# Kernel tuning notes

Measured on AMD Instinct MI355X. Metric: run time of the kernel, lower is better.

## Reference

```python
import jax, jax.numpy as jnp
import numpy as np

B, T, D, E = 4, 8192, 2048, 64


def setup_inputs() -> dict:
    key = jax.random.key(0)
    k1, k2 = jax.random.split(key)
    x = jax.random.normal(k1, (B, T, D), dtype=jnp.float32)
    kernel_DE = jax.random.normal(k2, (D, E), dtype=jnp.float32) * 0.02
    return {"x": x, "kernel_DE": kernel_DE, "num_experts_per_tok": 8}


def reference(x, kernel_DE, num_experts_per_tok):
    dtype = x.dtype
    # router logits: (B,T,E)
    router_logits_BTE = jnp.einsum("BTD,DE->BTE", x, kernel_DE)
    # gating probs in fp32 for numerical stability
    activated_gating_BTE = jax.nn.softmax(router_logits_BTE.astype(jnp.float32), axis=-1)
    # top-k experts per token
    weights_BTX, selected_experts_BTX = jax.lax.top_k(activated_gating_BTE, num_experts_per_tok)
    # renormalize selected weights via softmax in model dtype (faithful to source)
    normalized_weights_BTX = jax.nn.softmax(weights_BTX.astype(dtype), axis=-1)
    return (normalized_weights_BTX, selected_experts_BTX)
```

## Files before the change

### kernel.cpp

```cpp
#include <hip/hip_runtime.h>
#include <math.h>

#define NTOK  32768
#define DDIM  2048
#define NEXP  64
#define TOPK  8
#define GAP_THR  1e-4f
#define LIST_CAP 16384

#define WFRAG_OFF  1024
#define WFRAG_SZ   (64 * 4 * 2048)
#define LIST_OFF   (WFRAG_OFF + WFRAG_SZ)

#define CK      2
#define NCHUNK  (DDIM / 32 / CK)

typedef __attribute__((ext_vector_type(8))) short s8_t;
typedef __attribute__((ext_vector_type(4))) float f4_t;
typedef __attribute__((ext_vector_type(4))) unsigned int u4_t;

typedef const __attribute__((address_space(1))) unsigned int* as1p;
typedef __attribute__((address_space(3))) unsigned int* as3p;

__device__ __forceinline__ void gl2lds16(const void* g, void* l) {
  __builtin_amdgcn_global_load_lds((as1p)g, (as3p)l, 16, 0, 0);
}

__device__ __forceinline__ unsigned short f2bf(float f) {
  const unsigned u = __builtin_bit_cast(unsigned, f);
  const unsigned r = u + 0x7FFFu + ((u >> 16) & 1u);
  return (unsigned short)(r >> 16);
}

struct bfpair { unsigned hi, lo; };
__device__ __forceinline__ bfpair split2(float a, float b) {
  const unsigned ua = __builtin_bit_cast(unsigned, a);
  const unsigned ub = __builtin_bit_cast(unsigned, b);
  const unsigned ra = ua + 0x7FFFu + ((ua >> 16) & 1u);
  const unsigned rb = ub + 0x7FFFu + ((ub >> 16) & 1u);
  bfpair r;
  r.hi = (ra >> 16) | (rb & 0xFFFF0000u);
  const float fa = a - __builtin_bit_cast(float, ra & 0xFFFF0000u);
  const float fb = b - __builtin_bit_cast(float, rb & 0xFFFF0000u);
  r.lo = (__builtin_bit_cast(unsigned, fa) >> 16) |
         (__builtin_bit_cast(unsigned, fb) & 0xFFFF0000u);
  return r;
}

__global__ void wprep(const float* __restrict__ w, unsigned short* __restrict__ wf,
                      int* __restrict__ cnt) {
  if (blockIdx.x == 0 && threadIdx.x == 0) cnt[0] = 0;
  const int ks   = blockIdx.x;
  const int eg   = threadIdx.x >> 6;
  const int lane = threadIdx.x & 63;
  const int kb   = ks * 32 + ((lane >> 4) << 3);
  const int e    = (eg << 4) + (lane & 15);
  s8_t h, l;
#pragma unroll
  for (int j = 0; j < 8; ++j) {
    const float v = w[(size_t)(kb + j) * NEXP + e];
    const unsigned short hb = f2bf(v);
    const float hf = __builtin_bit_cast(float, (unsigned)hb << 16);
    h[j] = (short)hb;
    l[j] = (short)f2bf(v - hf);
  }
  unsigned short* base = wf + (size_t)(ks * 4 + eg) * 1024 + lane * 8;
  *(s8_t*)(base)       = h;
  *(s8_t*)(base + 512) = l;
}

__global__ __launch_bounds__(256, 2) void router_main(
    const float* __restrict__ x, const unsigned short* __restrict__ wfg,
    float* __restrict__ out, int* __restrict__ cnt, int* __restrict__ list) {
  __shared__ union {
    struct {
      float xb[2][4][CK * 512];
      unsigned short wb[2][CK * 4096];
    } s;
    float ll[64 * 68];
  } u;

  const int tid  = threadIdx.x;
  const int lane = tid & 63;
  const int wave = tid >> 6;
  const int col  = lane & 15;
  const int kgrp = lane >> 4;
  const int wtok = blockIdx.x * 64 + wave * 16;

  f4_t acc[4];
#pragma unroll
  for (int eg = 0; eg < 4; ++eg) acc[eg] = (f4_t){0.f, 0.f, 0.f, 0.f};

  const float* gx0 = x + (size_t)(wtok + col) * DDIM + (kgrp << 3);

  {
    float* lx = &u.s.xb[0][wave][0];
#pragma unroll
    for (int kk = 0; kk < CK; ++kk) {
      gl2lds16(gx0 + kk * 32,     lx + kk * 512);
      gl2lds16(gx0 + kk * 32 + 4, lx + kk * 512 + 256);
    }
    const unsigned short* gw = wfg + wave * 2048 + lane * 8;
    unsigned short* lw = &u.s.wb[0][wave * 2048];
#pragma unroll
    for (int j = 0; j < 4; ++j)
      gl2lds16(gw + j * 512, lw + j * 512);
  }
  __syncthreads();

#pragma unroll 1
  for (int c = 0; c < NCHUNK; ++c) {
    const int b = c & 1;
    if (c + 1 < NCHUNK) {
      const int nb = b ^ 1;
      const float* gx = gx0 + (size_t)((c + 1) * CK) * 32;
      float* lx = &u.s.xb[nb][wave][0];
#pragma unroll
      for (int kk = 0; kk < CK; ++kk) {
        gl2lds16(gx + kk * 32,     lx + kk * 512);
        gl2lds16(gx + kk * 32 + 4, lx + kk * 512 + 256);
      }
      const unsigned short* gw =
          wfg + (size_t)((c + 1) * CK) * 4096 + wave * 2048 + lane * 8;
      unsigned short* lw = &u.s.wb[nb][wave * 2048];
#pragma unroll
      for (int j = 0; j < 4; ++j)
        gl2lds16(gw + j * 512, lw + j * 512);
    }

    const float* lx = &u.s.xb[b][wave][0];
    const unsigned short* lw = &u.s.wb[b][0];
#pragma unroll
    for (int kk = 0; kk < CK; ++kk) {
      const float4 v0 = *(const float4*)(lx + kk * 512 + lane * 4);
      const float4 v1 = *(const float4*)(lx + kk * 512 + 256 + lane * 4);
      const bfpair p0 = split2(v0.x, v0.y);
      const bfpair p1 = split2(v0.z, v0.w);
      const bfpair p2 = split2(v1.x, v1.y);
      const bfpair p3 = split2(v1.z, v1.w);
      const u4_t uh = {p0.hi, p1.hi, p2.hi, p3.hi};
      const u4_t ul = {p0.lo, p1.lo, p2.lo, p3.lo};
      const s8_t ah = __builtin_bit_cast(s8_t, uh);
      const s8_t al = __builtin_bit_cast(s8_t, ul);
#pragma unroll
      for (int eg = 0; eg < 4; ++eg) {
        const s8_t bh = *(const s8_t*)(lw + kk * 4096 + eg * 1024 + lane * 8);
        const s8_t bl = *(const s8_t*)(lw + kk * 4096 + eg * 1024 + 512 + lane * 8);
        acc[eg] = __builtin_amdgcn_mfma_f32_16x16x32_bf16(ah, bh, acc[eg], 0, 0, 0);
        acc[eg] = __builtin_amdgcn_mfma_f32_16x16x32_bf16(al, bh, acc[eg], 0, 0, 0);
        acc[eg] = __builtin_amdgcn_mfma_f32_16x16x32_bf16(ah, bl, acc[eg], 0, 0, 0);
      }
    }
    __syncthreads();
  }

#pragma unroll
  for (int eg = 0; eg < 4; ++eg)
#pragma unroll
    for (int r = 0; r < 4; ++r)
      u.ll[(wave * 16 + kgrp * 4 + r) * 68 + eg * 16 + col] = acc[eg][r];
  __syncthreads();

  float* out_w = out;
  float* out_i = out + (size_t)NTOK * TOPK;

#pragma unroll 1
  for (int t = 0; t < 16; ++t) {
    const int tok = wtok + t;
    const float v = u.ll[(wave * 16 + t) * 68 + lane];

    float m = v;
#pragma unroll
    for (int off = 32; off; off >>= 1) m = fmaxf(m, __shfl_xor(m, off));
    const float ex = __expf(v - m);
    float s = ex;
#pragma unroll
    for (int off = 32; off; off >>= 1) s += __shfl_xor(s, off);
    float pw = ex / s;
    float lw = v;
    int   ii = lane;

    float selp[TOPK + 1];
    float sell[TOPK + 1];
    int   seli[TOPK + 1];
#pragma unroll
    for (int r = 0; r < TOPK + 1; ++r) {
      float bp = pw; float bl = lw; int bi = ii;
#pragma unroll
      for (int off = 32; off; off >>= 1) {
        const float op = __shfl_xor(bp, off);
        const float ol = __shfl_xor(bl, off);
        const int   oi = __shfl_xor(bi, off);
        const bool take = (op > bp) || (op == bp && oi < bi);
        bp = take ? op : bp;
        bl = take ? ol : bl;
        bi = take ? oi : bi;
      }
      selp[r] = bp; sell[r] = bl; seli[r] = bi;
      if (lane == bi) pw = -__builtin_inff();
    }

    bool contested = false;
#pragma unroll
    for (int k = 0; k < TOPK; ++k)
      contested |= (sell[k] - sell[k + 1]) <= GAP_THR;

    const float mm = selp[0];
    float ssum = 0.0f;
#pragma unroll
    for (int k = 0; k < TOPK; ++k) ssum += __expf(selp[k] - mm);
    float myv = selp[0];
    int   myi = seli[0];
#pragma unroll
    for (int k = 1; k < TOPK; ++k)
      if (lane == k) { myv = selp[k]; myi = seli[k]; }
    if (lane < TOPK) {
      out_w[(size_t)tok * TOPK + lane] = __expf(myv - mm) / ssum;
      out_i[(size_t)tok * TOPK + lane] = (float)myi;
    }

    if (contested && lane == 0) {
      const int idx = atomicAdd(cnt, 1);
      if (idx < LIST_CAP) list[idx] = tok;
    }
  }
}

__global__ __launch_bounds__(256, 1) void router_fix(
    const float* __restrict__ x, const float* __restrict__ w,
    float* __restrict__ out, const int* __restrict__ cnt,
    const int* __restrict__ list) {
  const int lane = threadIdx.x & 63;
  const int wave = threadIdx.x >> 6;
  const int gw   = blockIdx.x * 4 + wave;
  const int NW   = gridDim.x * 4;

  int n = cnt[0];
  if (n > LIST_CAP) n = LIST_CAP;

  float* out_w = out;
  float* out_i = out + (size_t)NTOK * TOPK;

  for (int i = gw; i < n; i += NW) {
    const int tok = list[i];
    const float* xr = x + (size_t)tok * DDIM;
    double a0 = 0.0, a1 = 0.0, a2 = 0.0, a3 = 0.0;
#pragma unroll 4
    for (int d4 = 0; d4 < DDIM / 4; ++d4) {
      const float4 xv = *(const float4*)(xr + d4 * 4);
      const int r = d4 * 4;
      a0 = fma((double)xv.x, (double)w[(r + 0) * NEXP + lane], a0);
      a1 = fma((double)xv.y, (double)w[(r + 1) * NEXP + lane], a1);
      a2 = fma((double)xv.z, (double)w[(r + 2) * NEXP + lane], a2);
      a3 = fma((double)xv.w, (double)w[(r + 3) * NEXP + lane], a3);
    }
    const double a = (a0 + a1) + (a2 + a3);

    double dm = a;
#pragma unroll
    for (int off = 32; off; off >>= 1) dm = fmax(dm, __shfl_xor(dm, off));
    const double dex = exp(a - dm);
    double ds = dex;
#pragma unroll
    for (int off = 32; off; off >>= 1) ds += __shfl_xor(ds, off);
    double dpv = dex / ds;

    double dselv[TOPK];
    int    dseli[TOPK];
#pragma unroll
    for (int r = 0; r < TOPK; ++r) {
      double bv = dpv;
      int    bi = lane;
#pragma unroll
      for (int off = 32; off; off >>= 1) {
        const double ov = __shfl_xor(bv, off);
        const int    oi = __shfl_xor(bi, off);
        const bool take = (ov > bv) || (ov == bv && oi < bi);
        bv = take ? ov : bv;
        bi = take ? oi : bi;
      }
      dselv[r] = bv;
      dseli[r] = bi;
      if (lane == bi) dpv = -1.0e300;
    }
    const double dmm = dselv[0];
    double dssum = 0.0;
#pragma unroll
    for (int k = 0; k < TOPK; ++k) dssum += exp(dselv[k] - dmm);
    double myv = dselv[0];
    int    myi = dseli[0];
#pragma unroll
    for (int k = 1; k < TOPK; ++k)
      if (lane == k) { myv = dselv[k]; myi = dseli[k]; }
    if (lane < TOPK) {
      out_w[(size_t)tok * TOPK + lane] = (float)(exp(myv - dmm) / dssum);
      out_i[(size_t)tok * TOPK + lane] = (float)myi;
    }
  }
}

extern "C" void kernel_launch(void* const* d_in, const int* in_sizes, int n_in,
                              void* d_out, int out_size, void* d_ws, size_t ws_size,
                              hipStream_t stream) {
  const float* x = (const float*)d_in[0];
  const float* w = (const float*)d_in[1];
  int* cnt = (int*)d_ws;
  unsigned short* wfrag = (unsigned short*)((char*)d_ws + WFRAG_OFF);
  int* list = (int*)((char*)d_ws + LIST_OFF);

  wprep<<<dim3(64), dim3(256), 0, stream>>>(w, wfrag, cnt);
  router_main<<<dim3(NTOK / 64), dim3(256), 0, stream>>>(
      x, wfrag, (float*)d_out, cnt, list);
  router_fix<<<dim3(256), dim3(256), 0, stream>>>(
      x, w, (float*)d_out, cnt, list);
}
```

Baseline: 531.3 us.

## Split K dimension across two wave halves with 512-thread blocks

Doubles the block to 8 waves, with two halves each covering half of the D reduction for the same 16-token tiles. Partial accumulators are combined through LDS, and the top-k epilogue is split so each wave handles 8 tokens. The pipeline uses explicit vmcnt waits and raw s_barrier instead of __syncthreads, one 32-wide K step per stage. The aim is more waves in flight to hide memory latency on this bandwidth-bound GEMV-like op, at the cost of an extra LDS reduction and more barriers.

```diff
diff --git a/kernel.cpp b/kernel.cpp
--- a/kernel.cpp
+++ b/kernel.cpp
@@ -12,8 +12,7 @@
 #define WFRAG_SZ   (64 * 4 * 2048)
 #define LIST_OFF   (WFRAG_OFF + WFRAG_SZ)
 
-#define CK      2
-#define NCHUNK  (DDIM / 32 / CK)
+#define NKS   32
 
 typedef __attribute__((ext_vector_type(8))) short s8_t;
 typedef __attribute__((ext_vector_type(4))) float f4_t;
@@ -69,13 +68,13 @@
   *(s8_t*)(base + 512) = l;
 }
 
-__global__ __launch_bounds__(256, 2) void router_main(
+__global__ __launch_bounds__(512, 4) void router_main(
     const float* __restrict__ x, const unsigned short* __restrict__ wfg,
     float* __restrict__ out, int* __restrict__ cnt, int* __restrict__ list) {
   __shared__ union {
     struct {
-      float xb[2][4][CK * 512];
-      unsigned short wb[2][CK * 4096];
+      float xb[2][8][512];
+      unsigned short wb[2][2][4096];
     } s;
     float ll[64 * 68];
   } u;
@@ -83,91 +82,94 @@
   const int tid  = threadIdx.x;
   const int lane = tid & 63;
   const int wave = tid >> 6;
+  const int pair = wave & 3;
+  const int half = wave >> 2;
   const int col  = lane & 15;
   const int kgrp = lane >> 4;
-  const int wtok = blockIdx.x * 64 + wave * 16;
+  const int tok0 = blockIdx.x * 64 + pair * 16;
 
   f4_t acc[4];
 #pragma unroll
   for (int eg = 0; eg < 4; ++eg) acc[eg] = (f4_t){0.f, 0.f, 0.f, 0.f};
 
-  const float* gx0 = x + (size_t)(wtok + col) * DDIM + (kgrp << 3);
-
-  {
-    float* lx = &u.s.xb[0][wave][0];
-#pragma unroll
-    for (int kk = 0; kk < CK; ++kk) {
-      gl2lds16(gx0 + kk * 32,     lx + kk * 512);
-      gl2lds16(gx0 + kk * 32 + 4, lx + kk * 512 + 256);
-    }
-    const unsigned short* gw = wfg + wave * 2048 + lane * 8;
-    unsigned short* lw = &u.s.wb[0][wave * 2048];
-#pragma unroll
-    for (int j = 0; j < 4; ++j)
-      gl2lds16(gw + j * 512, lw + j * 512);
-  }
+  const float* gx = x + (size_t)(tok0 + col) * DDIM + half * (NKS * 32) + (kgrp << 3);
+  const unsigned short* gw0 = wfg + pair * 1024 + lane * 8;
+
+  auto issue = [&](int j, int bb) {
+    gl2lds16(gx + j * 32,     &u.s.xb[bb][wave][0]);
+    gl2lds16(gx + j * 32 + 4, &u.s.xb[bb][wave][256]);
+    const unsigned short* g = gw0 + (size_t)(half * NKS + j) * 4096;
+    gl2lds16(g,       &u.s.wb[bb][half][pair * 1024]);
+    gl2lds16(g + 512, &u.s.wb[bb][half][pair * 1024 + 512]);
+  };
+
+  auto compute = [&](int bb) {
+    const float* lx = &u.s.xb[bb][wave][0];
+    const unsigned short* lw = &u.s.wb[bb][half][0];
+    const float4 v0 = *(const float4*)(lx + lane * 4);
+    const float4 v1 = *(const float4*)(lx + 256 + lane * 4);
+    const bfpair p0 = split2(v0.x, v0.y);
+    const bfpair p1 = split2(v0.z, v0.w);
+    const bfpair p2 = split2(v1.x, v1.y);
+    const bfpair p3 = split2(v1.z, v1.w);
+    const u4_t uh = {p0.hi, p1.hi, p2.hi, p3.hi};
+    const u4_t ul = {p0.lo, p1.lo, p2.lo, p3.lo};
+    const s8_t ah = __builtin_bit_cast(s8_t, uh);
+    const s8_t al = __builtin_bit_cast(s8_t, ul);
+#pragma unroll
+    for (int eg = 0; eg < 4; ++eg) {
+      const s8_t bh = *(const s8_t*)(lw + eg * 1024 + lane * 8);
+      const s8_t bl = *(const s8_t*)(lw + eg * 1024 + 512 + lane * 8);
+      acc[eg] = __builtin_amdgcn_mfma_f32_16x16x32_bf16(ah, bh, acc[eg], 0, 0, 0);
+      acc[eg] = __builtin_amdgcn_mfma_f32_16x16x32_bf16(al, bh, acc[eg], 0, 0, 0);
+      acc[eg] = __builtin_amdgcn_mfma_f32_16x16x32_bf16(ah, bl, acc[eg], 0, 0, 0);
+    }
+  };
+
+  issue(0, 0);
+
+#pragma unroll 1
+  for (int c = 0; c < NKS - 1; ++c) {
+    issue(c + 1, (c + 1) & 1);
+    asm volatile("s_waitcnt vmcnt(4)" ::: "memory");
+    __builtin_amdgcn_s_barrier();
+    asm volatile("" ::: "memory");
+    compute(c & 1);
+    asm volatile("" ::: "memory");
+    __builtin_amdgcn_s_barrier();
+  }
+  asm volatile("s_waitcnt vmcnt(0)" ::: "memory");
+  __builtin_amdgcn_s_barrier();
+  asm volatile("" ::: "memory");
+  compute((NKS - 1) & 1);
   __syncthreads();
 
-#pragma unroll 1
-  for (int c = 0; c < NCHUNK; ++c) {
-    const int b = c & 1;
-    if (c + 1 < NCHUNK) {
-      const int nb = b ^ 1;
-      const float* gx = gx0 + (size_t)((c + 1) * CK) * 32;
-      float* lx = &u.s.xb[nb][wave][0];
-#pragma unroll
-      for (int kk = 0; kk < CK; ++kk) {
-        gl2lds16(gx + kk * 32,     lx + kk * 512);
-        gl2lds16(gx + kk * 32 + 4, lx + kk * 512 + 256);
-      }
-      const unsigned short* gw =
-          wfg + (size_t)((c + 1) * CK) * 4096 + wave * 2048 + lane * 8;
-      unsigned short* lw = &u.s.wb[nb][wave * 2048];
-#pragma unroll
-      for (int j = 0; j < 4; ++j)
-        gl2lds16(gw + j * 512, lw + j * 512);
-    }
-
-    const float* lx = &u.s.xb[b][wave][0];
-    const unsigned short* lw = &u.s.wb[b][0];
-#pragma unroll
-    for (int kk = 0; kk < CK; ++kk) {
-      const float4 v0 = *(const float4*)(lx + kk * 512 + lane * 4);
-      const float4 v1 = *(const float4*)(lx + kk * 512 + 256 + lane * 4);
-      const bfpair p0 = split2(v0.x, v0.y);
-      const bfpair p1 = split2(v0.z, v0.w);
-      const bfpair p2 = split2(v1.x, v1.y);
-      const bfpair p3 = split2(v1.z, v1.w);
-      const u4_t uh = {p0.hi, p1.hi, p2.hi, p3.hi};
-      const u4_t ul = {p0.lo, p1.lo, p2.lo, p3.lo};
-      const s8_t ah = __builtin_bit_cast(s8_t, uh);
-      const s8_t al = __builtin_bit_cast(s8_t, ul);
-#pragma unroll
-      for (int eg = 0; eg < 4; ++eg) {
-        const s8_t bh = *(const s8_t*)(lw + kk * 4096 + eg * 1024 + lane * 8);
-        const s8_t bl = *(const s8_t*)(lw + kk * 4096 + eg * 1024 + 512 + lane * 8);
-        acc[eg] = __builtin_amdgcn_mfma_f32_16x16x32_bf16(ah, bh, acc[eg], 0, 0, 0);
-        acc[eg] = __builtin_amdgcn_mfma_f32_16x16x32_bf16(al, bh, acc[eg], 0, 0, 0);
-        acc[eg] = __builtin_amdgcn_mfma_f32_16x16x32_bf16(ah, bl, acc[eg], 0, 0, 0);
-      }
-    }
-    __syncthreads();
-  }
-
-#pragma unroll
-  for (int eg = 0; eg < 4; ++eg)
-#pragma unroll
-    for (int r = 0; r < 4; ++r)
-      u.ll[(wave * 16 + kgrp * 4 + r) * 68 + eg * 16 + col] = acc[eg][r];
+  if (half == 0) {
+#pragma unroll
+    for (int eg = 0; eg < 4; ++eg)
+#pragma unroll
+      for (int r = 0; r < 4; ++r)
+        u.ll[(pair * 16 + kgrp * 4 + r) * 68 + eg * 16 + col] = acc[eg][r];
+  }
+  __syncthreads();
+  if (half == 1) {
+#pragma unroll
+    for (int eg = 0; eg < 4; ++eg)
+#pragma unroll
+      for (int r = 0; r < 4; ++r)
+        u.ll[(pair * 16 + kgrp * 4 + r) * 68 + eg * 16 + col] += acc[eg][r];
+  }
   __syncthreads();
 
   float* out_w = out;
   float* out_i = out + (size_t)NTOK * TOPK;
 
+  const int trow0 = pair * 16 + half * 8;
 #pragma unroll 1
-  for (int t = 0; t < 16; ++t) {
-    const int tok = wtok + t;
-    const float v = u.ll[(wave * 16 + t) * 68 + lane];
+  for (int t = 0; t < 8; ++t) {
+    const int row = trow0 + t;
+    const int tok = blockIdx.x * 64 + row;
+    const float v = u.ll[row * 68 + lane];
 
     float m = v;
 #pragma unroll
@@ -309,7 +311,7 @@
   int* list = (int*)((char*)d_ws + LIST_OFF);
 
   wprep<<<dim3(64), dim3(256), 0, stream>>>(w, wfrag, cnt);
-  router_main<<<dim3(NTOK / 64), dim3(256), 0, stream>>>(
+  router_main<<<dim3(NTOK / 64), dim3(512), 0, stream>>>(
       x, wfrag, (float*)d_out, cnt, list);
   router_fix<<<dim3(256), dim3(256), 0, stream>>>(
       x, w, (float*)d_out, cnt, list);
```

New measurement: 529.1 us. Within noise of the previous version (-0.4%).
